# Optimization experiments

Measured on AMD Instinct MI355X. Metric: run time of the kernel, lower is better.

## Reference

```python
import jax, jax.numpy as jnp
import numpy as np

N = 100000   # nodes
C = 128      # in_channels
K = 32       # n_super_nodes
B = 64       # graphs (num segments)


def setup_inputs() -> dict:
    key = jax.random.key(0)
    k_x, k_b, k_w1, k_b1, k_w2, k_b2 = jax.random.split(key, 6)
    x = jax.random.normal(k_x, (N, C), dtype=jnp.float32)
    batch = jnp.sort(jax.random.randint(k_b, (N,), 0, B))
    # assign_mlp params: Linear(C,C) -> ReLU -> Linear(C,K); stored as [in,out]
    W1 = jax.random.normal(k_w1, (C, C), dtype=jnp.float32) / np.sqrt(C)
    b1 = jax.random.normal(k_b1, (C,), dtype=jnp.float32) * 0.01
    W2 = jax.random.normal(k_w2, (C, K), dtype=jnp.float32) / np.sqrt(C)
    b2 = jax.random.normal(k_b2, (K,), dtype=jnp.float32) * 0.01
    return {"x": x, "batch": batch, "W1": W1, "b1": b1, "W2": W2, "b2": b2}


def reference(x, batch, W1, b1, W2, b2):
    # assignment logits: MLP over node features
    h = jax.nn.relu(x @ W1 + b1)          # [N, C]
    s = jax.nn.softmax(h @ W2 + b2, axis=-1)  # [N, K]
    # outer product per node, then scatter-sum by graph id
    x_expanded = x[:, None, :] * s[:, :, None]  # [N, K, C]
    out = jax.ops.segment_sum(x_expanded, batch, num_segments=B)  # [B, K, C]
    return (out, s)
```

## Files before the change

kernel.cpp:

```cpp
#include <hip/hip_runtime.h>
#include <hip/hip_bf16.h>

#define NN 100000
#define CC 128
#define KK 32
#define BB 64
#define PS 16

typedef __bf16 bf16x8 __attribute__((ext_vector_type(8)));
typedef float  f32x4  __attribute__((ext_vector_type(4)));

__device__ __forceinline__ unsigned short f2bf(float v) {
    union { __bf16 h; unsigned short s; } u;
    u.h = (__bf16)v;
    return u.s;
}
__device__ __forceinline__ float bf2f(unsigned short h) {
    union { unsigned u; float f; } a; a.u = ((unsigned)h) << 16;
    return a.f;
}
__device__ __forceinline__ void unpack_hilo(uint4 a, uint4 b,
                                            bf16x8& hi8, bf16x8& lo8) {
    union { unsigned u[4]; bf16x8 v; } H, L;
    H.u[0] = __builtin_amdgcn_perm(a.y, a.x, 0x05040100u);
    H.u[1] = __builtin_amdgcn_perm(a.w, a.z, 0x05040100u);
    H.u[2] = __builtin_amdgcn_perm(b.y, b.x, 0x05040100u);
    H.u[3] = __builtin_amdgcn_perm(b.w, b.z, 0x05040100u);
    L.u[0] = __builtin_amdgcn_perm(a.y, a.x, 0x07060302u);
    L.u[1] = __builtin_amdgcn_perm(a.w, a.z, 0x07060302u);
    L.u[2] = __builtin_amdgcn_perm(b.y, b.x, 0x07060302u);
    L.u[3] = __builtin_amdgcn_perm(b.w, b.z, 0x07060302u);
    hi8 = H.v; lo8 = L.v;
}

__device__ __forceinline__ void atomAddF(float* p, float v) {
#if defined(__gfx950__) || defined(__gfx942__) || defined(__gfx90a__)
    unsafeAtomicAdd(p, v);
#else
    atomicAdd(p, v);
#endif
}

__global__ __launch_bounds__(256) void hp_prep(const int* __restrict__ batch,
                                               const float* __restrict__ W1,
                                               const float* __restrict__ W2,
                                               int* __restrict__ bounds,
                                               unsigned short* __restrict__ w1f,
                                               unsigned short* __restrict__ w2f,
                                               float* __restrict__ out_zero) {
    if (blockIdx.x == 0 && threadIdx.x <= BB) {
        const int b = threadIdx.x;
        int lo = 0, hi = NN;
        while (lo < hi) {
            const int mid = (lo + hi) >> 1;
            if (batch[mid] < b) lo = mid + 1; else hi = mid;
        }
        bounds[b] = lo;
    }
    const int t = blockIdx.x * 256 + threadIdx.x;
    {
        const int idx  = t;
        const int j    = idx & 7;
        const int lane = (idx >> 3) & 63;
        const int nt   = (idx >> 9) & 7;
        const int kt   = idx >> 12;
        const int k = kt * 32 + (lane >> 4) * 8 + j;
        const int n = nt * 16 + (lane & 15);
        const float w = W1[k * CC + n];
        const unsigned short h = f2bf(w);
        w1f[idx]         = h;
        w1f[16384 + idx] = f2bf(w - bf2f(h));
    }
    if (t < 4096) {
        const int idx  = t;
        const int j    = idx & 7;
        const int lane = (idx >> 3) & 63;
        const int nt   = (idx >> 9) & 1;
        const int kt   = idx >> 10;
        const int k = kt * 32 + (lane >> 4) * 8 + j;
        const int n = nt * 16 + (lane & 15);
        const float w = W2[k * KK + n];
        const unsigned short h = f2bf(w);
        w2f[idx]        = h;
        w2f[4096 + idx] = f2bf(w - bf2f(h));
    }
    const float4 z = make_float4(0.f, 0.f, 0.f, 0.f);
    #pragma unroll
    for (int i = t; i < BB * KK * CC / 4; i += 16384)
        *(float4*)(out_zero + (size_t)i * 4) = z;
}

__global__ __launch_bounds__(256, 6) void hp_mlp(
    const float* __restrict__ x,
    const unsigned short* __restrict__ w1f,
    const unsigned short* __restrict__ w2f,
    const float* __restrict__ b1,
    const float* __restrict__ b2,
    float* __restrict__ s_out,
    unsigned short* __restrict__ xb,
    unsigned short* __restrict__ sb)
{
    __shared__ __align__(16) char uni[16896];
    __shared__ float lgT[32][36];
    __shared__ float redm[4][32];
    __shared__ float reds[4][32];

    unsigned short* xa   = (unsigned short*)uni;
    unsigned int*   hs16 = (unsigned int*)uni;

    const int t    = threadIdx.x;
    const int wave = __builtin_amdgcn_readfirstlane(t >> 6);
    const int lane = t & 63;
    const int base = blockIdx.x * 32;

    #pragma unroll
    for (int mt = 0; mt < 2; ++mt) {
        const int q  = mt * 4 + wave;
        const int n  = base + mt * 16 + (lane & 15);
        const int ck = wave * 32 + (lane >> 4) * 8;
        const float4 va = *(const float4*)(x + (size_t)n * CC + ck);
        const float4 vb = *(const float4*)(x + (size_t)n * CC + ck + 4);
        const float v[8] = {va.x, va.y, va.z, va.w, vb.x, vb.y, vb.z, vb.w};
        union { unsigned short s[8]; uint4 u; } H, L;
        #pragma unroll
        for (int j = 0; j < 8; ++j) {
            H.s[j] = f2bf(v[j]);
            L.s[j] = f2bf(v[j] - bf2f(H.s[j]));
        }
        unsigned short* d0 = xa + (q * 64 + lane) * 8;
        *(uint4*)(d0)        = H.u;
        *(uint4*)(d0 + 4096) = L.u;
    }

    #pragma unroll
    for (int cc = 0; cc < 2; ++cc) {
        const int ct = wave * 2 + cc;
        const int c  = ct * 16 + (lane & 15);
        const int nb = base + (lane >> 4) * 8;
        union { unsigned short s[8]; uint4 u; } Hb;
        #pragma unroll
        for (int j = 0; j < 8; ++j)
            Hb.s[j] = f2bf(x[(size_t)(nb + j) * CC + c]);
        unsigned short* dp = xb + ((size_t)(blockIdx.x * 8 + ct) * 64 + lane) * 8;
        *(uint4*)dp = Hb.u;
    }
    __syncthreads();

    f32x4 acc[2][2];
    #pragma unroll
    for (int mt = 0; mt < 2; ++mt)
        #pragma unroll
        for (int nl = 0; nl < 2; ++nl)
            acc[mt][nl] = (f32x4){0.f, 0.f, 0.f, 0.f};

    #pragma unroll
    for (int kt = 0; kt < 4; ++kt) {
        bf16x8 ah[2], al[2];
        #pragma unroll
        for (int mt = 0; mt < 2; ++mt) {
            ah[mt] = *(const bf16x8*)(xa + ((mt * 4 + kt) * 64 + lane) * 8);
            al[mt] = *(const bf16x8*)(xa + 4096 + ((mt * 4 + kt) * 64 + lane) * 8);
        }
        #pragma unroll
        for (int nl = 0; nl < 2; ++nl) {
            const int nt = 2 * wave + nl;
            const bf16x8 wh = *(const bf16x8*)(w1f + ((kt * 8 + nt) * 64 + lane) * 8);
            const bf16x8 wl = *(const bf16x8*)(w1f + 16384 + ((kt * 8 + nt) * 64 + lane) * 8);
            #pragma unroll
            for (int mt = 0; mt < 2; ++mt) {
                acc[mt][nl] = __builtin_amdgcn_mfma_f32_16x16x32_bf16(ah[mt], wh, acc[mt][nl], 0, 0, 0);
                acc[mt][nl] = __builtin_amdgcn_mfma_f32_16x16x32_bf16(al[mt], wh, acc[mt][nl], 0, 0, 0);
                acc[mt][nl] = __builtin_amdgcn_mfma_f32_16x16x32_bf16(ah[mt], wl, acc[mt][nl], 0, 0, 0);
            }
        }
    }
    __syncthreads();

    #pragma unroll
    for (int nl = 0; nl < 2; ++nl) {
        const int c = (2 * wave + nl) * 16 + (lane & 15);
        const float bv = b1[c];
        #pragma unroll
        for (int mt = 0; mt < 2; ++mt)
            #pragma unroll
            for (int r = 0; r < 4; ++r) {
                const int node = mt * 16 + (lane >> 4) * 4 + r;
                const float h = fmaxf(acc[mt][nl][r] + bv, 0.f);
                const unsigned short hi = f2bf(h);
                const unsigned short lo = f2bf(h - bf2f(hi));
                hs16[node * 132 + c] = (unsigned)hi | ((unsigned)lo << 16);
            }
    }
    __syncthreads();

    {
        const int mt2 = wave & 1, nt2 = wave >> 1;
        f32x4 dacc = (f32x4){0.f, 0.f, 0.f, 0.f};
        #pragma unroll
        for (int kt = 0; kt < 4; ++kt) {
            const unsigned* hp = hs16 + (mt2 * 16 + (lane & 15)) * 132
                                      + kt * 32 + (lane >> 4) * 8;
            const uint4 u0 = *(const uint4*)hp;
            const uint4 u1 = *(const uint4*)(hp + 4);
            bf16x8 ah, al;
            unpack_hilo(u0, u1, ah, al);
            const bf16x8 wh = *(const bf16x8*)(w2f + ((kt * 2 + nt2) * 64 + lane) * 8);
            const bf16x8 wl = *(const bf16x8*)(w2f + 4096 + ((kt * 2 + nt2) * 64 + lane) * 8);
            dacc = __builtin_amdgcn_mfma_f32_16x16x32_bf16(ah, wh, dacc, 0, 0, 0);
            dacc = __builtin_amdgcn_mfma_f32_16x16x32_bf16(al, wh, dacc, 0, 0, 0);
            dacc = __builtin_amdgcn_mfma_f32_16x16x32_bf16(ah, wl, dacc, 0, 0, 0);
        }
        const int kcol = nt2 * 16 + (lane & 15);
        #pragma unroll
        for (int r = 0; r < 4; ++r) {
            const int node = mt2 * 16 + (lane >> 4) * 4 + r;
            lgT[node][kcol] = dacc[r];
        }
    }
    __syncthreads();

    const int node = lane & 31;
    const int koff = ((lane >> 5) << 4) + wave * 4;
    const float4 bv2 = *(const float4*)(b2 + koff);
    const float4 lv  = *(const float4*)&lgT[node][koff];
    float lg[4] = {lv.x + bv2.x, lv.y + bv2.y, lv.z + bv2.z, lv.w + bv2.w};

    float m = fmaxf(fmaxf(lg[0], lg[1]), fmaxf(lg[2], lg[3]));
    m = fmaxf(m, __shfl_xor(m, 32));
    if (lane < 32) redm[wave][lane] = m;
    __syncthreads();
    const float M = fmaxf(fmaxf(redm[0][node], redm[1][node]),
                          fmaxf(redm[2][node], redm[3][node]));
    const float e0 = __expf(lg[0] - M);
    const float e1 = __expf(lg[1] - M);
    const float e2 = __expf(lg[2] - M);
    const float e3 = __expf(lg[3] - M);
    float sp = (e0 + e1) + (e2 + e3);
    sp += __shfl_xor(sp, 32);
    if (lane < 32) reds[wave][lane] = sp;
    __syncthreads();
    const float S = (reds[0][node] + reds[1][node]) + (reds[2][node] + reds[3][node]);
    const float inv = 1.f / S;
    const float4 s4 = make_float4(e0 * inv, e1 * inv, e2 * inv, e3 * inv);
    *(float4*)(s_out + (size_t)(base + node) * KK + koff) = s4;
    *(float4*)&lgT[node][koff] = s4;
    __syncthreads();

    if (wave < 2) {
        const int k  = wave * 16 + (lane & 15);
        const int r0 = (lane >> 4) * 8;
        union { unsigned short s[8]; uint4 u; } V;
        #pragma unroll
        for (int j = 0; j < 8; ++j)
            V.s[j] = f2bf(lgT[r0 + j][k]);
        unsigned short* dp = sb + ((size_t)(blockIdx.x * 2 + wave) * 64 + lane) * 8;
        *(uint4*)dp = V.u;
    }
}

__global__ __launch_bounds__(256) void hp_pool(
    const unsigned short* __restrict__ xb,
    const unsigned short* __restrict__ sb,
    const int* __restrict__ bounds,
    float* __restrict__ out)
{
    const int b = blockIdx.x / PS;
    const int p = blockIdx.x - b * PS;
    const int wave = __builtin_amdgcn_readfirstlane(threadIdx.x >> 6);
    const int lane = threadIdx.x & 63;

    const int gs = bounds[b], ge = bounds[b + 1];
    const int c0g = gs >> 5;
    const int cnt = ((ge + 31) >> 5) - c0g;
    const int ch0 = c0g + (cnt * p) / PS;
    const int ch1 = c0g + (cnt * (p + 1)) / PS;

    const int mt    = wave & 1;
    const int chalf = wave >> 1;
    const int nrow  = (lane >> 4) * 8;

    f32x4 acc[4];
    #pragma unroll
    for (int i = 0; i < 4; ++i) acc[i] = (f32x4){0.f, 0.f, 0.f, 0.f};

    for (int ch = ch0; ch < ch1; ++ch) {
        union { uint4 u; unsigned short s[8]; bf16x8 v; } A;
        A.u = *(const uint4*)(sb + ((size_t)(ch * 2 + mt) * 64 + lane) * 8);
        const int nb = ch * 32 + nrow;
        #pragma unroll
        for (int j = 0; j < 8; ++j)
            if (nb + j < gs || nb + j >= ge) A.s[j] = 0;
        #pragma unroll
        for (int i = 0; i < 4; ++i) {
            const int ct = chalf * 4 + i;
            const bf16x8 Bv = *(const bf16x8*)(xb + ((size_t)(ch * 8 + ct) * 64 + lane) * 8);
            acc[i] = __builtin_amdgcn_mfma_f32_16x16x32_bf16(A.v, Bv, acc[i], 0, 0, 0);
        }
    }

    float* op = out + (size_t)b * KK * CC;
    #pragma unroll
    for (int i = 0; i < 4; ++i) {
        const int c = (chalf * 4 + i) * 16 + (lane & 15);
        #pragma unroll
        for (int r = 0; r < 4; ++r) {
            const int k = mt * 16 + (lane >> 4) * 4 + r;
            atomAddF(op + k * CC + c, acc[i][r]);
        }
    }
}

extern "C" void kernel_launch(void* const* d_in, const int* in_sizes, int n_in,
                              void* d_out, int out_size, void* d_ws, size_t ws_size,
                              hipStream_t stream) {
    const float* x     = (const float*)d_in[0];
    const int*   batch = (const int*)d_in[1];
    const float* W1    = (const float*)d_in[2];
    const float* b1    = (const float*)d_in[3];
    const float* W2    = (const float*)d_in[4];
    const float* b2    = (const float*)d_in[5];

    float* out = (float*)d_out;
    float* s   = out + (size_t)BB * KK * CC;

    char* ws = (char*)d_ws;
    int*            bounds = (int*)ws;
    unsigned short* w1f    = (unsigned short*)(ws + 1024);
    unsigned short* w2f    = (unsigned short*)(ws + 66560);
    unsigned short* xb     = (unsigned short*)(ws + 82944);
    unsigned short* sb     = (unsigned short*)(ws + 82944 + 25600000);

    hp_prep<<<64, 256, 0, stream>>>(batch, W1, W2, bounds, w1f, w2f, out);
    hp_mlp<<<NN / 32, 256, 0, stream>>>(x, w1f, w2f, b1, b2, s, xb, sb);
    hp_pool<<<BB * PS, 256, 0, stream>>>(xb, sb, bounds, out);
}
```

Before: 139.1 us.

## Fuse MLP and segment pooling into one kernel with per-block running accumulation

Merges the MLP/softmax kernel and the pooling kernel so each block processes four 32-node chunks. The bf16 x tile and the assignments stay in shared memory, and a per-graph MFMA accumulator is held in registers, flushed with atomics only when the graph id changes. This removes the global round trip of the bf16 x and s buffers, the bounds binary search and one launch. In exchange it runs fewer blocks at lower occupancy (launch bounds 3 instead of 6) and issues more atomic flushes, one per block per graph it touches.

New measurement: 132.9 us. -4.5%, faster.

```diff
diff --git a/kernel.cpp b/kernel.cpp
--- a/kernel.cpp
+++ b/kernel.cpp
@@ -5,7 +5,8 @@
 #define CC 128
 #define KK 32
 #define BB 64
-#define PS 16
+#define CH 4
+#define NCHUNK (NN / 32)
 
 typedef __bf16 bf16x8 __attribute__((ext_vector_type(8)));
 typedef float  f32x4  __attribute__((ext_vector_type(4)));
@@ -41,22 +42,11 @@
 #endif
 }
 
-__global__ __launch_bounds__(256) void hp_prep(const int* __restrict__ batch,
-                                               const float* __restrict__ W1,
+__global__ __launch_bounds__(256) void hp_prep(const float* __restrict__ W1,
                                                const float* __restrict__ W2,
-                                               int* __restrict__ bounds,
                                                unsigned short* __restrict__ w1f,
                                                unsigned short* __restrict__ w2f,
                                                float* __restrict__ out_zero) {
-    if (blockIdx.x == 0 && threadIdx.x <= BB) {
-        const int b = threadIdx.x;
-        int lo = 0, hi = NN;
-        while (lo < hi) {
-            const int mid = (lo + hi) >> 1;
-            if (batch[mid] < b) lo = mid + 1; else hi = mid;
-        }
-        bounds[b] = lo;
-    }
     const int t = blockIdx.x * 256 + threadIdx.x;
     {
         const int idx  = t;
@@ -85,22 +75,22 @@
         w2f[4096 + idx] = f2bf(w - bf2f(h));
     }
     const float4 z = make_float4(0.f, 0.f, 0.f, 0.f);
-    #pragma unroll
     for (int i = t; i < BB * KK * CC / 4; i += 16384)
         *(float4*)(out_zero + (size_t)i * 4) = z;
 }
 
-__global__ __launch_bounds__(256, 6) void hp_mlp(
+__global__ __launch_bounds__(256, 3) void hp_fused(
     const float* __restrict__ x,
     const unsigned short* __restrict__ w1f,
     const unsigned short* __restrict__ w2f,
     const float* __restrict__ b1,
     const float* __restrict__ b2,
+    const int* __restrict__ batch,
     float* __restrict__ s_out,
-    unsigned short* __restrict__ xb,
-    unsigned short* __restrict__ sb)
+    float* __restrict__ out)
 {
     __shared__ __align__(16) char uni[16896];
+    __shared__ __align__(16) unsigned short xbL[8 * 64 * 8];
     __shared__ float lgT[32][36];
     __shared__ float redm[4][32];
     __shared__ float reds[4][32];
@@ -111,203 +101,218 @@
     const int t    = threadIdx.x;
     const int wave = __builtin_amdgcn_readfirstlane(t >> 6);
     const int lane = t & 63;
-    const int base = blockIdx.x * 32;
-
-    #pragma unroll
-    for (int mt = 0; mt < 2; ++mt) {
-        const int q  = mt * 4 + wave;
-        const int n  = base + mt * 16 + (lane & 15);
-        const int ck = wave * 32 + (lane >> 4) * 8;
-        const float4 va = *(const float4*)(x + (size_t)n * CC + ck);
-        const float4 vb = *(const float4*)(x + (size_t)n * CC + ck + 4);
-        const float v[8] = {va.x, va.y, va.z, va.w, vb.x, vb.y, vb.z, vb.w};
-        union { unsigned short s[8]; uint4 u; } H, L;
-        #pragma unroll
-        for (int j = 0; j < 8; ++j) {
-            H.s[j] = f2bf(v[j]);
-            L.s[j] = f2bf(v[j] - bf2f(H.s[j]));
-        }
-        unsigned short* d0 = xa + (q * 64 + lane) * 8;
-        *(uint4*)(d0)        = H.u;
-        *(uint4*)(d0 + 4096) = L.u;
-    }
-
-    #pragma unroll
-    for (int cc = 0; cc < 2; ++cc) {
-        const int ct = wave * 2 + cc;
-        const int c  = ct * 16 + (lane & 15);
-        const int nb = base + (lane >> 4) * 8;
-        union { unsigned short s[8]; uint4 u; } Hb;
-        #pragma unroll
-        for (int j = 0; j < 8; ++j)
-            Hb.s[j] = f2bf(x[(size_t)(nb + j) * CC + c]);
-        unsigned short* dp = xb + ((size_t)(blockIdx.x * 8 + ct) * 64 + lane) * 8;
-        *(uint4*)dp = Hb.u;
-    }
-    __syncthreads();
-
-    f32x4 acc[2][2];
-    #pragma unroll
-    for (int mt = 0; mt < 2; ++mt)
-        #pragma unroll
-        for (int nl = 0; nl < 2; ++nl)
-            acc[mt][nl] = (f32x4){0.f, 0.f, 0.f, 0.f};
-
-    #pragma unroll
-    for (int kt = 0; kt < 4; ++kt) {
-        bf16x8 ah[2], al[2];
-        #pragma unroll
-        for (int mt = 0; mt < 2; ++mt) {
-            ah[mt] = *(const bf16x8*)(xa + ((mt * 4 + kt) * 64 + lane) * 8);
-            al[mt] = *(const bf16x8*)(xa + 4096 + ((mt * 4 + kt) * 64 + lane) * 8);
-        }
-        #pragma unroll
-        for (int nl = 0; nl < 2; ++nl) {
-            const int nt = 2 * wave + nl;
-            const bf16x8 wh = *(const bf16x8*)(w1f + ((kt * 8 + nt) * 64 + lane) * 8);
-            const bf16x8 wl = *(const bf16x8*)(w1f + 16384 + ((kt * 8 + nt) * 64 + lane) * 8);
-            #pragma unroll
-            for (int mt = 0; mt < 2; ++mt) {
-                acc[mt][nl] = __builtin_amdgcn_mfma_f32_16x16x32_bf16(ah[mt], wh, acc[mt][nl], 0, 0, 0);
-                acc[mt][nl] = __builtin_amdgcn_mfma_f32_16x16x32_bf16(al[mt], wh, acc[mt][nl], 0, 0, 0);
-                acc[mt][nl] = __builtin_amdgcn_mfma_f32_16x16x32_bf16(ah[mt], wl, acc[mt][nl], 0, 0, 0);
-            }
-        }
-    }
-    __syncthreads();
-
-    #pragma unroll
-    for (int nl = 0; nl < 2; ++nl) {
-        const int c = (2 * wave + nl) * 16 + (lane & 15);
-        const float bv = b1[c];
-        #pragma unroll
-        for (int mt = 0; mt < 2; ++mt)
-            #pragma unroll
-            for (int r = 0; r < 4; ++r) {
-                const int node = mt * 16 + (lane >> 4) * 4 + r;
-                const float h = fmaxf(acc[mt][nl][r] + bv, 0.f);
-                const unsigned short hi = f2bf(h);
-                const unsigned short lo = f2bf(h - bf2f(hi));
-                hs16[node * 132 + c] = (unsigned)hi | ((unsigned)lo << 16);
-            }
-    }
-    __syncthreads();
-
-    {
-        const int mt2 = wave & 1, nt2 = wave >> 1;
-        f32x4 dacc = (f32x4){0.f, 0.f, 0.f, 0.f};
-        #pragma unroll
-        for (int kt = 0; kt < 4; ++kt) {
-            const unsigned* hp = hs16 + (mt2 * 16 + (lane & 15)) * 132
-                                      + kt * 32 + (lane >> 4) * 8;
-            const uint4 u0 = *(const uint4*)hp;
-            const uint4 u1 = *(const uint4*)(hp + 4);
-            bf16x8 ah, al;
-            unpack_hilo(u0, u1, ah, al);
-            const bf16x8 wh = *(const bf16x8*)(w2f + ((kt * 2 + nt2) * 64 + lane) * 8);
-            const bf16x8 wl = *(const bf16x8*)(w2f + 4096 + ((kt * 2 + nt2) * 64 + lane) * 8);
-            dacc = __builtin_amdgcn_mfma_f32_16x16x32_bf16(ah, wh, dacc, 0, 0, 0);
-            dacc = __builtin_amdgcn_mfma_f32_16x16x32_bf16(al, wh, dacc, 0, 0, 0);
-            dacc = __builtin_amdgcn_mfma_f32_16x16x32_bf16(ah, wl, dacc, 0, 0, 0);
-        }
-        const int kcol = nt2 * 16 + (lane & 15);
-        #pragma unroll
-        for (int r = 0; r < 4; ++r) {
-            const int node = mt2 * 16 + (lane >> 4) * 4 + r;
-            lgT[node][kcol] = dacc[r];
-        }
-    }
-    __syncthreads();
-
-    const int node = lane & 31;
-    const int koff = ((lane >> 5) << 4) + wave * 4;
-    const float4 bv2 = *(const float4*)(b2 + koff);
-    const float4 lv  = *(const float4*)&lgT[node][koff];
-    float lg[4] = {lv.x + bv2.x, lv.y + bv2.y, lv.z + bv2.z, lv.w + bv2.w};
-
-    float m = fmaxf(fmaxf(lg[0], lg[1]), fmaxf(lg[2], lg[3]));
-    m = fmaxf(m, __shfl_xor(m, 32));
-    if (lane < 32) redm[wave][lane] = m;
-    __syncthreads();
-    const float M = fmaxf(fmaxf(redm[0][node], redm[1][node]),
-                          fmaxf(redm[2][node], redm[3][node]));
-    const float e0 = __expf(lg[0] - M);
-    const float e1 = __expf(lg[1] - M);
-    const float e2 = __expf(lg[2] - M);
-    const float e3 = __expf(lg[3] - M);
-    float sp = (e0 + e1) + (e2 + e3);
-    sp += __shfl_xor(sp, 32);
-    if (lane < 32) reds[wave][lane] = sp;
-    __syncthreads();
-    const float S = (reds[0][node] + reds[1][node]) + (reds[2][node] + reds[3][node]);
-    const float inv = 1.f / S;
-    const float4 s4 = make_float4(e0 * inv, e1 * inv, e2 * inv, e3 * inv);
-    *(float4*)(s_out + (size_t)(base + node) * KK + koff) = s4;
-    *(float4*)&lgT[node][koff] = s4;
-    __syncthreads();
-
-    if (wave < 2) {
-        const int k  = wave * 16 + (lane & 15);
-        const int r0 = (lane >> 4) * 8;
-        union { unsigned short s[8]; uint4 u; } V;
-        #pragma unroll
-        for (int j = 0; j < 8; ++j)
-            V.s[j] = f2bf(lgT[r0 + j][k]);
-        unsigned short* dp = sb + ((size_t)(blockIdx.x * 2 + wave) * 64 + lane) * 8;
-        *(uint4*)dp = V.u;
-    }
-}
-
-__global__ __launch_bounds__(256) void hp_pool(
-    const unsigned short* __restrict__ xb,
-    const unsigned short* __restrict__ sb,
-    const int* __restrict__ bounds,
-    float* __restrict__ out)
-{
-    const int b = blockIdx.x / PS;
-    const int p = blockIdx.x - b * PS;
-    const int wave = __builtin_amdgcn_readfirstlane(threadIdx.x >> 6);
-    const int lane = threadIdx.x & 63;
-
-    const int gs = bounds[b], ge = bounds[b + 1];
-    const int c0g = gs >> 5;
-    const int cnt = ((ge + 31) >> 5) - c0g;
-    const int ch0 = c0g + (cnt * p) / PS;
-    const int ch1 = c0g + (cnt * (p + 1)) / PS;
-
-    const int mt    = wave & 1;
+
+    const int pmt   = wave & 1;
     const int chalf = wave >> 1;
     const int nrow  = (lane >> 4) * 8;
 
-    f32x4 acc[4];
+    f32x4 pacc[4];
     #pragma unroll
-    for (int i = 0; i < 4; ++i) acc[i] = (f32x4){0.f, 0.f, 0.f, 0.f};
-
-    for (int ch = ch0; ch < ch1; ++ch) {
-        union { uint4 u; unsigned short s[8]; bf16x8 v; } A;
-        A.u = *(const uint4*)(sb + ((size_t)(ch * 2 + mt) * 64 + lane) * 8);
-        const int nb = ch * 32 + nrow;
-        #pragma unroll
-        for (int j = 0; j < 8; ++j)
-            if (nb + j < gs || nb + j >= ge) A.s[j] = 0;
+    for (int i = 0; i < 4; ++i) pacc[i] = (f32x4){0.f, 0.f, 0.f, 0.f};
+
+    int cg = __builtin_amdgcn_readfirstlane(batch[blockIdx.x * (CH * 32)]);
+
+    auto flush = [&](int g) {
+        float* op = out + (size_t)g * KK * CC;
         #pragma unroll
         for (int i = 0; i < 4; ++i) {
-            const int ct = chalf * 4 + i;
-            const bf16x8 Bv = *(const bf16x8*)(xb + ((size_t)(ch * 8 + ct) * 64 + lane) * 8);
-            acc[i] = __builtin_amdgcn_mfma_f32_16x16x32_bf16(A.v, Bv, acc[i], 0, 0, 0);
+            const int c = (chalf * 4 + i) * 16 + (lane & 15);
+            #pragma unroll
+            for (int r = 0; r < 4; ++r) {
+                const int k = pmt * 16 + (lane >> 4) * 4 + r;
+                atomAddF(op + k * CC + c, pacc[i][r]);
+            }
+            pacc[i] = (f32x4){0.f, 0.f, 0.f, 0.f};
+        }
+    };
+
+    #pragma unroll 1
+    for (int ch = 0; ch < CH; ++ch) {
+        const int chunk = blockIdx.x * CH + ch;
+        if (chunk >= NCHUNK) break;
+        const int base = chunk * 32;
+
+        __syncthreads();
+
+        #pragma unroll
+        for (int mt = 0; mt < 2; ++mt) {
+            const int q  = mt * 4 + wave;
+            const int n  = base + mt * 16 + (lane & 15);
+            const int ck = wave * 32 + (lane >> 4) * 8;
+            const float4 va = *(const float4*)(x + (size_t)n * CC + ck);
+            const float4 vb = *(const float4*)(x + (size_t)n * CC + ck + 4);
+            const float v[8] = {va.x, va.y, va.z, va.w, vb.x, vb.y, vb.z, vb.w};
+            union { unsigned short s[8]; uint4 u; } H, L;
+            #pragma unroll
+            for (int j = 0; j < 8; ++j) {
+                H.s[j] = f2bf(v[j]);
+                L.s[j] = f2bf(v[j] - bf2f(H.s[j]));
+            }
+            unsigned short* d0 = xa + (q * 64 + lane) * 8;
+            *(uint4*)(d0)        = H.u;
+            *(uint4*)(d0 + 4096) = L.u;
+        }
+
+        #pragma unroll
+        for (int cc = 0; cc < 2; ++cc) {
+            const int ct = wave * 2 + cc;
+            const int c  = ct * 16 + (lane & 15);
+            const int nb = base + nrow;
+            union { unsigned short s[8]; uint4 u; } Hb;
+            #pragma unroll
+            for (int j = 0; j < 8; ++j)
+                Hb.s[j] = f2bf(x[(size_t)(nb + j) * CC + c]);
+            *(uint4*)(xbL + ((size_t)ct * 64 + lane) * 8) = Hb.u;
+        }
+        __syncthreads();
+
+        f32x4 acc[2][2];
+        #pragma unroll
+        for (int mt = 0; mt < 2; ++mt)
+            #pragma unroll
+            for (int nl = 0; nl < 2; ++nl)
+                acc[mt][nl] = (f32x4){0.f, 0.f, 0.f, 0.f};
+
+        #pragma unroll
+        for (int kt = 0; kt < 4; ++kt) {
+            bf16x8 ah[2], al[2];
+            #pragma unroll
+            for (int mt = 0; mt < 2; ++mt) {
+                ah[mt] = *(const bf16x8*)(xa + ((mt * 4 + kt) * 64 + lane) * 8);
+                al[mt] = *(const bf16x8*)(xa + 4096 + ((mt * 4 + kt) * 64 + lane) * 8);
+            }
+            #pragma unroll
+            for (int nl = 0; nl < 2; ++nl) {
+                const int nt = 2 * wave + nl;
+                const bf16x8 wh = *(const bf16x8*)(w1f + ((kt * 8 + nt) * 64 + lane) * 8);
+                const bf16x8 wl = *(const bf16x8*)(w1f + 16384 + ((kt * 8 + nt) * 64 + lane) * 8);
+                #pragma unroll
+                for (int mt = 0; mt < 2; ++mt) {
+                    acc[mt][nl] = __builtin_amdgcn_mfma_f32_16x16x32_bf16(ah[mt], wh, acc[mt][nl], 0, 0, 0);
+                    acc[mt][nl] = __builtin_amdgcn_mfma_f32_16x16x32_bf16(al[mt], wh, acc[mt][nl], 0, 0, 0);
+                    acc[mt][nl] = __builtin_amdgcn_mfma_f32_16x16x32_bf16(ah[mt], wl, acc[mt][nl], 0, 0, 0);
+                }
+            }
+        }
+        __syncthreads();
+
+        #pragma unroll
+        for (int nl = 0; nl < 2; ++nl) {
+            const int c = (2 * wave + nl) * 16 + (lane & 15);
+            const float bv = b1[c];
+            #pragma unroll
+            for (int mt = 0; mt < 2; ++mt)
+                #pragma unroll
+                for (int r = 0; r < 4; ++r) {
+                    const int node = mt * 16 + (lane >> 4) * 4 + r;
+                    const float h = fmaxf(acc[mt][nl][r] + bv, 0.f);
+                    const unsigned short hi = f2bf(h);
+                    const unsigned short lo = f2bf(h - bf2f(hi));
+                    hs16[node * 132 + c] = (unsigned)hi | ((unsigned)lo << 16);
+                }
+        }
+        __syncthreads();
+
+        {
+            const int mt2 = wave & 1, nt2 = wave >> 1;
+            f32x4 dacc = (f32x4){0.f, 0.f, 0.f, 0.f};
+            #pragma unroll
+            for (int kt = 0; kt < 4; ++kt) {
+                const unsigned* hp = hs16 + (mt2 * 16 + (lane & 15)) * 132
+                                          + kt * 32 + (lane >> 4) * 8;
+                const uint4 u0 = *(const uint4*)hp;
+                const uint4 u1 = *(const uint4*)(hp + 4);
+                bf16x8 ah, al;
+                unpack_hilo(u0, u1, ah, al);
+                const bf16x8 wh = *(const bf16x8*)(w2f + ((kt * 2 + nt2) * 64 + lane) * 8);
+                const bf16x8 wl = *(const bf16x8*)(w2f + 4096 + ((kt * 2 + nt2) * 64 + lane) * 8);
+                dacc = __builtin_amdgcn_mfma_f32_16x16x32_bf16(ah, wh, dacc, 0, 0, 0);
+                dacc = __builtin_amdgcn_mfma_f32_16x16x32_bf16(al, wh, dacc, 0, 0, 0);
+                dacc = __builtin_amdgcn_mfma_f32_16x16x32_bf16(ah, wl, dacc, 0, 0, 0);
+            }
+            const int kcol = nt2 * 16 + (lane & 15);
+            #pragma unroll
+            for (int r = 0; r < 4; ++r) {
+                const int node = mt2 * 16 + (lane >> 4) * 4 + r;
+                lgT[node][kcol] = dacc[r];
+            }
+        }
+        __syncthreads();
+
+        {
+            const int node = lane & 31;
+            const int koff = ((lane >> 5) << 4) + wave * 4;
+            const float4 bv2 = *(const float4*)(b2 + koff);
+            const float4 lv  = *(const float4*)&lgT[node][koff];
+            float lg[4] = {lv.x + bv2.x, lv.y + bv2.y, lv.z + bv2.z, lv.w + bv2.w};
+
+            float m = fmaxf(fmaxf(lg[0], lg[1]), fmaxf(lg[2], lg[3]));
+            m = fmaxf(m, __shfl_xor(m, 32));
+            if (lane < 32) redm[wave][lane] = m;
+            __syncthreads();
+            const float M = fmaxf(fmaxf(redm[0][node], redm[1][node]),
+                                  fmaxf(redm[2][node], redm[3][node]));
+            const float e0 = __expf(lg[0] - M);
+            const float e1 = __expf(lg[1] - M);
+            const float e2 = __expf(lg[2] - M);
+            const float e3 = __expf(lg[3] - M);
+            float sp = (e0 + e1) + (e2 + e3);
+            sp += __shfl_xor(sp, 32);
+            if (lane < 32) reds[wave][lane] = sp;
+            __syncthreads();
+            const float S = (reds[0][node] + reds[1][node]) + (reds[2][node] + reds[3][node]);
+            const float inv = 1.f / S;
+            const float4 s4 = make_float4(e0 * inv, e1 * inv, e2 * inv, e3 * inv);
+            *(float4*)(s_out + (size_t)(base + node) * KK + koff) = s4;
+            *(float4*)&lgT[node][koff] = s4;
+        }
+        __syncthreads();
+
+        {
+            union { unsigned short s[8]; bf16x8 v; } A;
+            const int kA = pmt * 16 + (lane & 15);
+            #pragma unroll
+            for (int j = 0; j < 8; ++j)
+                A.s[j] = f2bf(lgT[nrow + j][kA]);
+            bf16x8 Bv[4];
+            #pragma unroll
+            for (int i = 0; i < 4; ++i)
+                Bv[i] = *(const bf16x8*)(xbL + ((size_t)(chalf * 4 + i) * 64 + lane) * 8);
+
+            const int gl0 = __builtin_amdgcn_readfirstlane(batch[base]);
+            const int gh  = __builtin_amdgcn_readfirstlane(batch[base + 31]);
+
+            if (gl0 == cg && gh == cg) {
+                #pragma unroll
+                for (int i = 0; i < 4; ++i)
+                    pacc[i] = __builtin_amdgcn_mfma_f32_16x16x32_bf16(A.v, Bv[i], pacc[i], 0, 0, 0);
+            } else {
+                int bt[8];
+                #pragma unroll
+                for (int j = 0; j < 8; ++j) bt[j] = batch[base + nrow + j];
+                while (cg < gh) {
+                    union { unsigned short s[8]; bf16x8 v; } Am;
+                    #pragma unroll
+                    for (int j = 0; j < 8; ++j)
+                        Am.s[j] = (bt[j] == cg) ? A.s[j] : (unsigned short)0;
+                    #pragma unroll
+                    for (int i = 0; i < 4; ++i)
+                        pacc[i] = __builtin_amdgcn_mfma_f32_16x16x32_bf16(Am.v, Bv[i], pacc[i], 0, 0, 0);
+                    flush(cg);
+                    ++cg;
+                }
+                union { unsigned short s[8]; bf16x8 v; } Am;
+                #pragma unroll
+                for (int j = 0; j < 8; ++j)
+                    Am.s[j] = (bt[j] == cg) ? A.s[j] : (unsigned short)0;
+                #pragma unroll
+                for (int i = 0; i < 4; ++i)
+                    pacc[i] = __builtin_amdgcn_mfma_f32_16x16x32_bf16(Am.v, Bv[i], pacc[i], 0, 0, 0);
+            }
         }
     }
 
-    float* op = out + (size_t)b * KK * CC;
-    #pragma unroll
-    for (int i = 0; i < 4; ++i) {
-        const int c = (chalf * 4 + i) * 16 + (lane & 15);
-        #pragma unroll
-        for (int r = 0; r < 4; ++r) {
-            const int k = mt * 16 + (lane >> 4) * 4 + r;
-            atomAddF(op + k * CC + c, acc[i][r]);
-        }
-    }
+    flush(cg);
 }
 
 extern "C" void kernel_launch(void* const* d_in, const int* in_sizes, int n_in,
@@ -324,13 +329,10 @@
     float* s   = out + (size_t)BB * KK * CC;
 
     char* ws = (char*)d_ws;
-    int*            bounds = (int*)ws;
-    unsigned short* w1f    = (unsigned short*)(ws + 1024);
-    unsigned short* w2f    = (unsigned short*)(ws + 66560);
-    unsigned short* xb     = (unsigned short*)(ws + 82944);
-    unsigned short* sb     = (unsigned short*)(ws + 82944 + 25600000);
-
-    hp_prep<<<64, 256, 0, stream>>>(batch, W1, W2, bounds, w1f, w2f, out);
-    hp_mlp<<<NN / 32, 256, 0, stream>>>(x, w1f, w2f, b1, b2, s, xb, sb);
-    hp_pool<<<BB * PS, 256, 0, stream>>>(xb, sb, bounds, out);
-}
+    unsigned short* w1f = (unsigned short*)ws;
+    unsigned short* w2f = (unsigned short*)(ws + 65536);
+
+    hp_prep<<<64, 256, 0, stream>>>(W1, W2, w1f, w2f, out);
+    const int nblk = (NCHUNK + CH - 1) / CH;
+    hp_fused<<<nblk, 256, 0, stream>>>(x, w1f, w2f, b1, b2, batch, s, out);
+}
```
